# Kernel optimization log

Measured on AMD Instinct MI355X. Metric: run time of the kernel, lower is better.

The kernel has to match this reference:

```python
import jax, jax.numpy as jnp
import numpy as np

N, E, DI, DO = 50000, 800000, 64, 64
EPS = 1e-06


def setup_inputs() -> dict:
    key = jax.random.key(0)
    ks = jax.random.split(key, 8)
    # xavier_uniform bounds: sqrt(6/(fan_in+fan_out))
    bf_f = float(np.sqrt(6.0 / (2 * DI + DO)))
    bf_w = float(np.sqrt(6.0 / (2 * DI + 1)))
    return {
        "x": jax.random.normal(ks[0], (N, DI), dtype=jnp.float32),
        "adj": jnp.zeros((1,), dtype=jnp.float32),  # unused in forward
        "src": jax.random.randint(ks[1], (E,), 0, N),
        "tgt": jax.random.randint(ks[2], (E,), 0, N),
        "Msrc": jnp.zeros((1,), dtype=jnp.float32),  # unused in forward
        "Wf": jax.random.uniform(ks[3], (DO, 2 * DI), jnp.float32, -bf_f, bf_f),
        "bf": jnp.zeros((DO,), dtype=jnp.float32),
        "Ww": jax.random.uniform(ks[4], (1, 2 * DI), jnp.float32, -bf_w, bf_w),
        "bw": jnp.zeros((1,), dtype=jnp.float32),
    }


def reference(x, adj, src, tgt, Msrc, Wf, bf, Ww, bw):
    n_nodes = x.shape[0]
    # edge gather + concat: h is [E, 2*di]
    h = jnp.concatenate([x[src], x[tgt]], axis=1)
    y = jax.nn.relu(h @ Wf.T + bf)          # [E, do]
    a = h @ Ww.T + bw                        # [E, 1]
    # Mtgt @ v  ==  segment_sum(v, tgt) since Mtgt is the target one-hot matrix
    a_sum = jax.ops.segment_sum(a, tgt, num_segments=n_nodes) + EPS   # [N, 1]
    o = jax.ops.segment_sum(y * a, tgt, num_segments=n_nodes) / a_sum  # [N, do]
    return o
```

## Files before the change

kernel.cpp:

```cpp
#include <hip/hip_runtime.h>
#include <hip/hip_bf16.h>


#define NBLK 200

__global__ __launch_bounds__(256) void gat_pre_hist(
    const float* __restrict__ x, const float* __restrict__ Wf,
    const float* __restrict__ Ww, const float* __restrict__ bf,
    const float* __restrict__ bw,
    __hip_bfloat16* __restrict__ A16, float* __restrict__ B,
    float* __restrict__ cg, float* __restrict__ dg, int N,
    const int* __restrict__ tgt, int* __restrict__ counts,
    int E, int NB, int chunk, int nb1)
{
    __shared__ float w2[64][132];
    __shared__ float xs[64][68];
    __shared__ float ww[128];
    __shared__ float bfs[64];
    __shared__ int   h[256];

    const int tid = threadIdx.x;

    if (blockIdx.x >= nb1) {
        const int k = blockIdx.x - nb1;
        h[tid] = 0;
        __syncthreads();
        const int lo = k * chunk;
        const int hi = min(lo + chunk, E);
        for (int e = lo + tid; e < hi; e += 256)
            atomicAdd(&h[tgt[e] >> 8], 1);
        __syncthreads();
        if (tid < NB) counts[tid * NBLK + k] = h[tid];
        return;
    }

    for (int f = tid; f < 64 * 128; f += 256) {
        int d  = f >> 7;
        int kk = f & 127;
        w2[kk & 63][(kk >> 6) * 64 + d] = Wf[f];
    }
    if (tid < 128) ww[tid] = Ww[tid];
    if (tid < 64)  bfs[tid] = bf[tid];

    const int n0 = blockIdx.x << 6;
    for (int i = tid; i < 64 * 64; i += 256) {
        int nl = i >> 6, k = i & 63;
        int n = n0 + nl;
        xs[k][nl] = (n < N) ? x[(size_t)n * 64 + k] : 0.f;
    }
    __syncthreads();

    const int ti = tid & 15, tj = tid >> 4;
    float acc[4][8];
#pragma unroll
    for (int i = 0; i < 4; ++i)
#pragma unroll
        for (int j = 0; j < 8; ++j) acc[i][j] = 0.f;

#pragma unroll 4
    for (int k = 0; k < 64; ++k) {
        const float4 xv = *(const float4*)&xs[k][ti * 4];
        const float4 w0 = *(const float4*)&w2[k][tj * 8];
        const float4 w1 = *(const float4*)&w2[k][tj * 8 + 4];
        const float xa[4] = {xv.x, xv.y, xv.z, xv.w};
        const float wa[8] = {w0.x, w0.y, w0.z, w0.w, w1.x, w1.y, w1.z, w1.w};
#pragma unroll
        for (int i = 0; i < 4; ++i)
#pragma unroll
            for (int j = 0; j < 8; ++j)
                acc[i][j] = fmaf(xa[i], wa[j], acc[i][j]);
    }

#pragma unroll
    for (int i = 0; i < 4; ++i) {
        const int n = n0 + ti * 4 + i;
        if (n < N) {
            if (tj < 8) {
#pragma unroll
                for (int j = 0; j < 8; ++j)
                    A16[(size_t)n * 64 + tj * 8 + j] = __float2bfloat16(acc[i][j]);
            } else {
#pragma unroll
                for (int j = 0; j < 8; ++j) {
                    int d2 = (tj - 8) * 8 + j;
                    B[(size_t)n * 64 + d2] = acc[i][j] + bfs[d2];
                }
            }
        }
    }

    if (tid < 64) {
        const int n = n0 + tid;
        if (n < N) {
            float sc = 0.f, sd = 0.f;
            for (int k = 0; k < 64; ++k) {
                const float xv = xs[k][tid];
                sc = fmaf(xv, ww[k], sc);
                sd = fmaf(xv, ww[64 + k], sd);
            }
            cg[n] = sc;
            dg[n] = sd + bw[0];
        }
    }
}

__global__ __launch_bounds__(256) void gat_scan1(
    const int* __restrict__ in, int* __restrict__ out,
    int* __restrict__ bsum, int n)
{
    __shared__ int tmp[256];
    const int i = blockIdx.x * 256 + threadIdx.x;
    const int v = (i < n) ? in[i] : 0;
    tmp[threadIdx.x] = v;
    __syncthreads();
#pragma unroll
    for (int off = 1; off < 256; off <<= 1) {
        const int add = (threadIdx.x >= off) ? tmp[threadIdx.x - off] : 0;
        __syncthreads();
        tmp[threadIdx.x] += add;
        __syncthreads();
    }
    if (i < n) out[i] = tmp[threadIdx.x] - v;
    if (threadIdx.x == 255) bsum[blockIdx.x] = tmp[255];
}

__global__ __launch_bounds__(1024) void gat_scan2(int* __restrict__ bsum, int nb)
{
    __shared__ int tmp[1024];
    const int v = (threadIdx.x < nb) ? bsum[threadIdx.x] : 0;
    tmp[threadIdx.x] = v;
    __syncthreads();
#pragma unroll
    for (int off = 1; off < 1024; off <<= 1) {
        const int add = (threadIdx.x >= off) ? tmp[threadIdx.x - off] : 0;
        __syncthreads();
        tmp[threadIdx.x] += add;
        __syncthreads();
    }
    if (threadIdx.x < nb) bsum[threadIdx.x] = tmp[threadIdx.x] - v;
}

__global__ __launch_bounds__(256) void gat_partition(
    const int* __restrict__ src, const int* __restrict__ tgt,
    const int* __restrict__ counts, const int* __restrict__ bsum,
    unsigned int* __restrict__ pairs, int E, int NB, int chunk)
{
    __shared__ int cur[256];
    const int k = blockIdx.x;
    const int tid = threadIdx.x;
    if (tid < NB) {
        const int idx = tid * NBLK + k;
        cur[tid] = counts[idx] + bsum[idx >> 8];
    }
    __syncthreads();
    const int lo = k * chunk;
    const int hi = min(lo + chunk, E);
    for (int e = lo + tid; e < hi; e += 256) {
        const int t = tgt[e];
        const int s = src[e];
        const int pos = atomicAdd(&cur[t >> 8], 1);
        pairs[pos] = ((unsigned int)s << 8) | (unsigned int)(t & 255);
    }
}

__global__ __launch_bounds__(256) void gat_bucket_sort(
    const unsigned int* __restrict__ pairs, const int* __restrict__ counts,
    const int* __restrict__ bsum,
    int* __restrict__ starts, int* __restrict__ sorted_src,
    int N, int E, int NB)
{
    __shared__ int h[256];
    __shared__ int cur[256];
    const int b = blockIdx.x;
    const int tid = threadIdx.x;
    const int i0 = b * NBLK;
    const int base = counts[i0] + bsum[i0 >> 8];
    int end = E;
    if (b + 1 < NB) {
        const int i1 = (b + 1) * NBLK;
        end = counts[i1] + bsum[i1 >> 8];
    }

    h[tid] = 0;
    __syncthreads();
    for (int e = base + tid; e < end; e += 256)
        atomicAdd(&h[pairs[e] & 255u], 1);
    __syncthreads();
    const int v = h[tid];
#pragma unroll
    for (int off = 1; off < 256; off <<= 1) {
        const int add = (tid >= off) ? h[tid - off] : 0;
        __syncthreads();
        h[tid] += add;
        __syncthreads();
    }
    const int excl = h[tid] - v;
    const int node = (b << 8) + tid;
    if (node < N) starts[node] = base + excl;
    if (b == NB - 1 && tid == 0) starts[N] = E;
    cur[tid] = base + excl;
    __syncthreads();
    for (int e = base + tid; e < end; e += 256) {
        const unsigned int p = pairs[e];
        const int pos = atomicAdd(&cur[p & 255u], 1);
        sorted_src[pos] = (int)(p >> 8);
    }
}

__global__ __launch_bounds__(256) void gat_gather(
    const int* __restrict__ starts, const int* __restrict__ sorted_src,
    const __hip_bfloat16* __restrict__ A16, const float* __restrict__ B,
    const float* __restrict__ cg, const float* __restrict__ dg,
    float* __restrict__ out, int N)
{
    const int d = threadIdx.x & 63;
    const int node = blockIdx.x * (blockDim.x >> 6) + (threadIdx.x >> 6);
    if (node >= N) return;
    const int e0 = starts[node];
    const int e1 = starts[node + 1];
    const float Bt  = B[(size_t)node * 64 + d];
    const float dgt = dg[node];
    float acc = 0.f, asum = 0.f;

    int e = e0;
    for (; e + 7 < e1; e += 8) {
        int s[8];
#pragma unroll
        for (int u = 0; u < 8; ++u) s[u] = sorted_src[e + u];
        float a[8], xv[8];
#pragma unroll
        for (int u = 0; u < 8; ++u) a[u] = cg[s[u]] + dgt;
#pragma unroll
        for (int u = 0; u < 8; ++u)
            xv[u] = __bfloat162float(A16[(size_t)s[u] * 64 + d]);
#pragma unroll
        for (int u = 0; u < 8; ++u) {
            acc = fmaf(fmaxf(xv[u] + Bt, 0.f), a[u], acc);
            asum += a[u];
        }
    }
    for (; e + 3 < e1; e += 4) {
        const int s0 = sorted_src[e];
        const int s1 = sorted_src[e + 1];
        const int s2 = sorted_src[e + 2];
        const int s3 = sorted_src[e + 3];
        const float a0 = cg[s0] + dgt;
        const float a1 = cg[s1] + dgt;
        const float a2 = cg[s2] + dgt;
        const float a3 = cg[s3] + dgt;
        const float x0 = __bfloat162float(A16[(size_t)s0 * 64 + d]);
        const float x1 = __bfloat162float(A16[(size_t)s1 * 64 + d]);
        const float x2 = __bfloat162float(A16[(size_t)s2 * 64 + d]);
        const float x3 = __bfloat162float(A16[(size_t)s3 * 64 + d]);
        acc = fmaf(fmaxf(x0 + Bt, 0.f), a0, acc);
        acc = fmaf(fmaxf(x1 + Bt, 0.f), a1, acc);
        acc = fmaf(fmaxf(x2 + Bt, 0.f), a2, acc);
        acc = fmaf(fmaxf(x3 + Bt, 0.f), a3, acc);
        asum += (a0 + a1) + (a2 + a3);
    }
    for (; e < e1; ++e) {
        const int s   = sorted_src[e];
        const float a = cg[s] + dgt;
        const float xv = __bfloat162float(A16[(size_t)s * 64 + d]);
        acc = fmaf(fmaxf(xv + Bt, 0.f), a, acc);
        asum += a;
    }
    out[(size_t)node * 64 + d] = acc / (asum + 1e-6f);
}

extern "C" void kernel_launch(void* const* d_in, const int* in_sizes, int n_in,
                              void* d_out, int out_size, void* d_ws, size_t ws_size,
                              hipStream_t stream)
{
    const float* x   = (const float*)d_in[0];
    const int*   src = (const int*)d_in[2];
    const int*   tgt = (const int*)d_in[3];
    const float* Wf  = (const float*)d_in[5];
    const float* bf  = (const float*)d_in[6];
    const float* Ww  = (const float*)d_in[7];
    const float* bw  = (const float*)d_in[8];

    const int N = in_sizes[0] / 64;
    const int E = in_sizes[2];
    float* out = (float*)d_out;

    const int NB    = (N + 255) >> 8;
    const int chunk = (E + NBLK - 1) / NBLK;
    const int NBNB  = NB * NBLK;

    unsigned int* pairs = (unsigned int*)d_out;

    __hip_bfloat16* A16 = (__hip_bfloat16*)d_ws;
    float* B          = (float*)(A16 + (size_t)N * 64);
    float* cg         = B + (size_t)N * 64;
    float* dg         = cg + N;
    int*   starts     = (int*)(dg + N);
    int*   sorted_src = starts + N + 1;
    int*   counts     = sorted_src + E;
    int*   bsum       = counts + NBNB;

    const int nb1 = (N + 63) / 64;
    gat_pre_hist<<<nb1 + NBLK, 256, 0, stream>>>(x, Wf, Ww, bf, bw, A16, B, cg, dg, N,
                                                 tgt, counts, E, NB, chunk, nb1);
    const int nbs = (NBNB + 255) / 256;
    gat_scan1<<<nbs, 256, 0, stream>>>(counts, counts, bsum, NBNB);
    gat_scan2<<<1, 1024, 0, stream>>>(bsum, nbs);
    gat_partition<<<NBLK, 256, 0, stream>>>(src, tgt, counts, bsum, pairs, E, NB, chunk);
    gat_bucket_sort<<<NB, 256, 0, stream>>>(pairs, counts, bsum, starts, sorted_src, N, E, NB);
    const int nb2 = (N + 3) / 4;
    gat_gather<<<nb2, 256, 0, stream>>>(starts, sorted_src, A16, B, cg, dg, out, N);
}
```

Baseline: 88.46 us.

## Fuse bucket sort with gather using LDS-resident per-bucket edge lists

Merges the per-bucket counting sort and the neighbor gather into one kernel. Each bucket of 256 target nodes is sorted in LDS together with its attention coefficients, then four blocks per bucket each redo the sort and handle 64 nodes. Buckets larger than a fixed capacity fall back to a global buffer. B is now stored in the output buffer and pairs moves to the workspace, which removes the sorted_src and starts round trips through global memory and one launch. The cost is that every bucket's histogram and sort is done four times, and the large LDS allocation lowers occupancy.

```diff
diff --git a/kernel.cpp b/kernel.cpp
--- a/kernel.cpp
+++ b/kernel.cpp
@@ -3,6 +3,8 @@
 
 
 #define NBLK 200
+#define CAP  5120
+#define GSPLIT 4
 
 __global__ __launch_bounds__(256) void gat_pre_hist(
     const float* __restrict__ x, const float* __restrict__ Wf,
@@ -163,16 +165,23 @@
     }
 }
 
-__global__ __launch_bounds__(256) void gat_bucket_sort(
+__global__ __launch_bounds__(256) void gat_sort_gather(
     const unsigned int* __restrict__ pairs, const int* __restrict__ counts,
-    const int* __restrict__ bsum,
-    int* __restrict__ starts, int* __restrict__ sorted_src,
-    int N, int E, int NB)
-{
-    __shared__ int h[256];
-    __shared__ int cur[256];
-    const int b = blockIdx.x;
+    const int* __restrict__ bsum, int* __restrict__ gfb,
+    const __hip_bfloat16* __restrict__ A16,
+    const float* __restrict__ cg, const float* __restrict__ dg,
+    float* __restrict__ out, int N, int E, int NB)
+{
+    __shared__ int   h[256];
+    __shared__ int   cur[256];
+    __shared__ int   nstart[257];
+    __shared__ int   s_lds[CAP];
+    __shared__ float ae_lds[CAP];
+
+    const int b   = blockIdx.x / GSPLIT;
+    const int sl  = blockIdx.x % GSPLIT;
     const int tid = threadIdx.x;
+
     const int i0 = b * NBLK;
     const int base = counts[i0] + bsum[i0 >> 8];
     int end = E;
@@ -180,6 +189,8 @@
         const int i1 = (b + 1) * NBLK;
         end = counts[i1] + bsum[i1 >> 8];
     }
+    const int cnt = end - base;
+    const bool fits = (cnt <= CAP);
 
     h[tid] = 0;
     __syncthreads();
@@ -195,77 +206,70 @@
         __syncthreads();
     }
     const int excl = h[tid] - v;
-    const int node = (b << 8) + tid;
-    if (node < N) starts[node] = base + excl;
-    if (b == NB - 1 && tid == 0) starts[N] = E;
-    cur[tid] = base + excl;
-    __syncthreads();
-    for (int e = base + tid; e < end; e += 256) {
-        const unsigned int p = pairs[e];
-        const int pos = atomicAdd(&cur[p & 255u], 1);
-        sorted_src[pos] = (int)(p >> 8);
-    }
-}
-
-__global__ __launch_bounds__(256) void gat_gather(
-    const int* __restrict__ starts, const int* __restrict__ sorted_src,
-    const __hip_bfloat16* __restrict__ A16, const float* __restrict__ B,
-    const float* __restrict__ cg, const float* __restrict__ dg,
-    float* __restrict__ out, int N)
-{
-    const int d = threadIdx.x & 63;
-    const int node = blockIdx.x * (blockDim.x >> 6) + (threadIdx.x >> 6);
-    if (node >= N) return;
-    const int e0 = starts[node];
-    const int e1 = starts[node + 1];
-    const float Bt  = B[(size_t)node * 64 + d];
-    const float dgt = dg[node];
-    float acc = 0.f, asum = 0.f;
-
-    int e = e0;
-    for (; e + 7 < e1; e += 8) {
-        int s[8];
-#pragma unroll
-        for (int u = 0; u < 8; ++u) s[u] = sorted_src[e + u];
-        float a[8], xv[8];
-#pragma unroll
-        for (int u = 0; u < 8; ++u) a[u] = cg[s[u]] + dgt;
-#pragma unroll
-        for (int u = 0; u < 8; ++u)
-            xv[u] = __bfloat162float(A16[(size_t)s[u] * 64 + d]);
-#pragma unroll
-        for (int u = 0; u < 8; ++u) {
-            acc = fmaf(fmaxf(xv[u] + Bt, 0.f), a[u], acc);
-            asum += a[u];
-        }
-    }
-    for (; e + 3 < e1; e += 4) {
-        const int s0 = sorted_src[e];
-        const int s1 = sorted_src[e + 1];
-        const int s2 = sorted_src[e + 2];
-        const int s3 = sorted_src[e + 3];
-        const float a0 = cg[s0] + dgt;
-        const float a1 = cg[s1] + dgt;
-        const float a2 = cg[s2] + dgt;
-        const float a3 = cg[s3] + dgt;
-        const float x0 = __bfloat162float(A16[(size_t)s0 * 64 + d]);
-        const float x1 = __bfloat162float(A16[(size_t)s1 * 64 + d]);
-        const float x2 = __bfloat162float(A16[(size_t)s2 * 64 + d]);
-        const float x3 = __bfloat162float(A16[(size_t)s3 * 64 + d]);
-        acc = fmaf(fmaxf(x0 + Bt, 0.f), a0, acc);
-        acc = fmaf(fmaxf(x1 + Bt, 0.f), a1, acc);
-        acc = fmaf(fmaxf(x2 + Bt, 0.f), a2, acc);
-        acc = fmaf(fmaxf(x3 + Bt, 0.f), a3, acc);
-        asum += (a0 + a1) + (a2 + a3);
-    }
-    for (; e < e1; ++e) {
-        const int s   = sorted_src[e];
-        const float a = cg[s] + dgt;
-        const float xv = __bfloat162float(A16[(size_t)s * 64 + d]);
-        acc = fmaf(fmaxf(xv + Bt, 0.f), a, acc);
-        asum += a;
-    }
-    out[(size_t)node * 64 + d] = acc / (asum + 1e-6f);
+    nstart[tid] = excl;
+    if (tid == 0) nstart[256] = cnt;
+    cur[tid] = excl;
+    __syncthreads();
+
+    if (fits) {
+        for (int e = base + tid; e < end; e += 256) {
+            const unsigned int p = pairs[e];
+            const int pos = atomicAdd(&cur[p & 255u], 1);
+            const int s = (int)(p >> 8);
+            s_lds[pos]  = s;
+            ae_lds[pos] = cg[s];
+        }
+    } else {
+        for (int e = base + tid; e < end; e += 256) {
+            const unsigned int p = pairs[e];
+            const int pos = atomicAdd(&cur[p & 255u], 1);
+            gfb[base + pos] = (int)(p >> 8);
+        }
+    }
+    __syncthreads();
+
+    const int d = tid & 63;
+    const int w = tid >> 6;
+    for (int i = 0; i < 16; ++i) {
+        const int nl = sl * 64 + w * 16 + i;
+        const int node = (b << 8) + nl;
+        if (node >= N) continue;
+        const int e0 = nstart[nl];
+        const int e1 = nstart[nl + 1];
+        const float Bt  = out[(size_t)node * 64 + d];
+        const float dgt = dg[node];
+        float acc = 0.f, asum = 0.f;
+        if (fits) {
+            int e = e0;
+            for (; e + 7 < e1; e += 8) {
+                int sv[8]; float av[8];
+#pragma unroll
+                for (int u = 0; u < 8; ++u) { sv[u] = s_lds[e + u]; av[u] = ae_lds[e + u] + dgt; }
+#pragma unroll
+                for (int u = 0; u < 8; ++u) {
+                    const float xv = __bfloat162float(A16[(size_t)sv[u] * 64 + d]);
+                    acc = fmaf(fmaxf(xv + Bt, 0.f), av[u], acc);
+                    asum += av[u];
+                }
+            }
+            for (; e < e1; ++e) {
+                const int s = s_lds[e];
+                const float a = ae_lds[e] + dgt;
+                const float xv = __bfloat162float(A16[(size_t)s * 64 + d]);
+                acc = fmaf(fmaxf(xv + Bt, 0.f), a, acc);
+                asum += a;
+            }
+        } else {
+            for (int e = e0; e < e1; ++e) {
+                const int s = gfb[base + e];
+                const float a = cg[s] + dgt;
+                const float xv = __bfloat162float(A16[(size_t)s * 64 + d]);
+                acc = fmaf(fmaxf(xv + Bt, 0.f), a, acc);
+                asum += a;
+            }
+        }
+        out[(size_t)node * 64 + d] = acc / (asum + 1e-6f);
+    }
 }
 
 extern "C" void kernel_launch(void* const* d_in, const int* in_sizes, int n_in,
@@ -288,16 +292,15 @@
     const int chunk = (E + NBLK - 1) / NBLK;
     const int NBNB  = NB * NBLK;
 
-    unsigned int* pairs = (unsigned int*)d_out;
+    float* B = out;
 
     __hip_bfloat16* A16 = (__hip_bfloat16*)d_ws;
-    float* B          = (float*)(A16 + (size_t)N * 64);
-    float* cg         = B + (size_t)N * 64;
+    float* cg         = (float*)(A16 + (size_t)N * 64);
     float* dg         = cg + N;
-    int*   starts     = (int*)(dg + N);
-    int*   sorted_src = starts + N + 1;
-    int*   counts     = sorted_src + E;
+    int*   gfb        = (int*)(dg + N);
+    int*   counts     = gfb + E;
     int*   bsum       = counts + NBNB;
+    unsigned int* pairs = (unsigned int*)(bsum + 1024);
 
     const int nb1 = (N + 63) / 64;
     gat_pre_hist<<<nb1 + NBLK, 256, 0, stream>>>(x, Wf, Ww, bf, bw, A16, B, cg, dg, N,
@@ -306,7 +309,6 @@
     gat_scan1<<<nbs, 256, 0, stream>>>(counts, counts, bsum, NBNB);
     gat_scan2<<<1, 1024, 0, stream>>>(bsum, nbs);
     gat_partition<<<NBLK, 256, 0, stream>>>(src, tgt, counts, bsum, pairs, E, NB, chunk);
-    gat_bucket_sort<<<NB, 256, 0, stream>>>(pairs, counts, bsum, starts, sorted_src, N, E, NB);
-    const int nb2 = (N + 3) / 4;
-    gat_gather<<<nb2, 256, 0, stream>>>(starts, sorted_src, A16, B, cg, dg, out, N);
-}
+    gat_sort_gather<<<NB * GSPLIT, 256, 0, stream>>>(pairs, counts, bsum, gfb,
+                                                     A16, cg, dg, out, N, E, NB);
+}
```

New measurement: 147.0 us. 66.2% more time.

## Precompute per-edge attention in bucket sort and store B in output buffer

Applied to the files above, without the earlier changes.

The bucket sort now looks up cg[src] once per edge and writes a packed (src, a) int2, so the gather loop no longer does a dependent random load of cg per edge. B is moved into the output buffer, where each thread reads its own element before overwriting it, and pairs move to workspace. The bucket sort now runs 1024 threads per block, and the gather drops its 4-wide tail loop. This doubles the sorted-array traffic and adds a random cg read inside the sort kernel.

```diff
diff --git a/kernel.cpp b/kernel.cpp
--- a/kernel.cpp
+++ b/kernel.cpp
@@ -163,10 +163,10 @@
     }
 }
 
-__global__ __launch_bounds__(256) void gat_bucket_sort(
+__global__ __launch_bounds__(1024) void gat_bucket_sort(
     const unsigned int* __restrict__ pairs, const int* __restrict__ counts,
-    const int* __restrict__ bsum,
-    int* __restrict__ starts, int* __restrict__ sorted_src,
+    const int* __restrict__ bsum, const float* __restrict__ cg,
+    int* __restrict__ starts, int2* __restrict__ sorted_sa,
     int N, int E, int NB)
 {
     __shared__ int h[256];
@@ -181,36 +181,40 @@
         end = counts[i1] + bsum[i1 >> 8];
     }
 
-    h[tid] = 0;
-    __syncthreads();
-    for (int e = base + tid; e < end; e += 256)
+    if (tid < 256) h[tid] = 0;
+    __syncthreads();
+    for (int e = base + tid; e < end; e += 1024)
         atomicAdd(&h[pairs[e] & 255u], 1);
     __syncthreads();
-    const int v = h[tid];
+    const int v = (tid < 256) ? h[tid] : 0;
 #pragma unroll
     for (int off = 1; off < 256; off <<= 1) {
-        const int add = (tid >= off) ? h[tid - off] : 0;
-        __syncthreads();
-        h[tid] += add;
-        __syncthreads();
-    }
-    const int excl = h[tid] - v;
-    const int node = (b << 8) + tid;
-    if (node < N) starts[node] = base + excl;
-    if (b == NB - 1 && tid == 0) starts[N] = E;
-    cur[tid] = base + excl;
-    __syncthreads();
-    for (int e = base + tid; e < end; e += 256) {
+        int add = 0;
+        if (tid < 256 && tid >= off) add = h[tid - off];
+        __syncthreads();
+        if (tid < 256) h[tid] += add;
+        __syncthreads();
+    }
+    if (tid < 256) {
+        const int excl = h[tid] - v;
+        const int node = (b << 8) + tid;
+        if (node < N) starts[node] = base + excl;
+        if (b == NB - 1 && tid == 0) starts[N] = E;
+        cur[tid] = base + excl;
+    }
+    __syncthreads();
+    for (int e = base + tid; e < end; e += 1024) {
         const unsigned int p = pairs[e];
+        const int s = (int)(p >> 8);
+        const float ae = cg[s];
         const int pos = atomicAdd(&cur[p & 255u], 1);
-        sorted_src[pos] = (int)(p >> 8);
+        sorted_sa[pos] = make_int2(s, __float_as_int(ae));
     }
 }
 
 __global__ __launch_bounds__(256) void gat_gather(
-    const int* __restrict__ starts, const int* __restrict__ sorted_src,
-    const __hip_bfloat16* __restrict__ A16, const float* __restrict__ B,
-    const float* __restrict__ cg, const float* __restrict__ dg,
+    const int* __restrict__ starts, const int2* __restrict__ sorted_sa,
+    const __hip_bfloat16* __restrict__ A16, const float* __restrict__ dg,
     float* __restrict__ out, int N)
 {
     const int d = threadIdx.x & 63;
@@ -218,50 +222,30 @@
     if (node >= N) return;
     const int e0 = starts[node];
     const int e1 = starts[node + 1];
-    const float Bt  = B[(size_t)node * 64 + d];
+    const float Bt  = out[(size_t)node * 64 + d];
     const float dgt = dg[node];
     float acc = 0.f, asum = 0.f;
 
     int e = e0;
     for (; e + 7 < e1; e += 8) {
-        int s[8];
-#pragma unroll
-        for (int u = 0; u < 8; ++u) s[u] = sorted_src[e + u];
-        float a[8], xv[8];
-#pragma unroll
-        for (int u = 0; u < 8; ++u) a[u] = cg[s[u]] + dgt;
+        int2 sa[8];
+#pragma unroll
+        for (int u = 0; u < 8; ++u) sa[u] = sorted_sa[e + u];
+        float xv[8];
 #pragma unroll
         for (int u = 0; u < 8; ++u)
-            xv[u] = __bfloat162float(A16[(size_t)s[u] * 64 + d]);
+            xv[u] = __bfloat162float(A16[(size_t)sa[u].x * 64 + d]);
 #pragma unroll
         for (int u = 0; u < 8; ++u) {
-            acc = fmaf(fmaxf(xv[u] + Bt, 0.f), a[u], acc);
-            asum += a[u];
+            const float a = __int_as_float(sa[u].y) + dgt;
+            acc = fmaf(fmaxf(xv[u] + Bt, 0.f), a, acc);
+            asum += a;
         }
     }
-    for (; e + 3 < e1; e += 4) {
-        const int s0 = sorted_src[e];
-        const int s1 = sorted_src[e + 1];
-        const int s2 = sorted_src[e + 2];
-        const int s3 = sorted_src[e + 3];
-        const float a0 = cg[s0] + dgt;
-        const float a1 = cg[s1] + dgt;
-        const float a2 = cg[s2] + dgt;
-        const float a3 = cg[s3] + dgt;
-        const float x0 = __bfloat162float(A16[(size_t)s0 * 64 + d]);
-        const float x1 = __bfloat162float(A16[(size_t)s1 * 64 + d]);
-        const float x2 = __bfloat162float(A16[(size_t)s2 * 64 + d]);
-        const float x3 = __bfloat162float(A16[(size_t)s3 * 64 + d]);
-        acc = fmaf(fmaxf(x0 + Bt, 0.f), a0, acc);
-        acc = fmaf(fmaxf(x1 + Bt, 0.f), a1, acc);
-        acc = fmaf(fmaxf(x2 + Bt, 0.f), a2, acc);
-        acc = fmaf(fmaxf(x3 + Bt, 0.f), a3, acc);
-        asum += (a0 + a1) + (a2 + a3);
-    }
     for (; e < e1; ++e) {
-        const int s   = sorted_src[e];
-        const float a = cg[s] + dgt;
-        const float xv = __bfloat162float(A16[(size_t)s * 64 + d]);
+        const int2 sa = sorted_sa[e];
+        const float a = __int_as_float(sa.y) + dgt;
+        const float xv = __bfloat162float(A16[(size_t)sa.x * 64 + d]);
         acc = fmaf(fmaxf(xv + Bt, 0.f), a, acc);
         asum += a;
     }
@@ -288,15 +272,15 @@
     const int chunk = (E + NBLK - 1) / NBLK;
     const int NBNB  = NB * NBLK;
 
-    unsigned int* pairs = (unsigned int*)d_out;
+    float* B = out;
 
     __hip_bfloat16* A16 = (__hip_bfloat16*)d_ws;
-    float* B          = (float*)(A16 + (size_t)N * 64);
-    float* cg         = B + (size_t)N * 64;
+    int2*  sorted_sa  = (int2*)(A16 + (size_t)N * 64);
+    unsigned int* pairs = (unsigned int*)(sorted_sa + E);
+    float* cg         = (float*)(pairs + E);
     float* dg         = cg + N;
     int*   starts     = (int*)(dg + N);
-    int*   sorted_src = starts + N + 1;
-    int*   counts     = sorted_src + E;
+    int*   counts     = starts + N + 1;
     int*   bsum       = counts + NBNB;
 
     const int nb1 = (N + 63) / 64;
@@ -306,7 +290,8 @@
     gat_scan1<<<nbs, 256, 0, stream>>>(counts, counts, bsum, NBNB);
     gat_scan2<<<1, 1024, 0, stream>>>(bsum, nbs);
     gat_partition<<<NBLK, 256, 0, stream>>>(src, tgt, counts, bsum, pairs, E, NB, chunk);
-    gat_bucket_sort<<<NB, 256, 0, stream>>>(pairs, counts, bsum, starts, sorted_src, N, E, NB);
+    gat_bucket_sort<<<NB, 1024, 0, stream>>>(pairs, counts, bsum, cg,
+                                             starts, sorted_sa, N, E, NB);
     const int nb2 = (N + 3) / 4;
-    gat_gather<<<nb2, 256, 0, stream>>>(starts, sorted_src, A16, B, cg, dg, out, N);
-}
+    gat_gather<<<nb2, 256, 0, stream>>>(starts, sorted_sa, A16, dg, out, N);
+}
```

Result: slower. 93.66 us (+5.9%).
